# Kernel optimization log

Hardware: AMD Instinct MI355X
Metric: run time of the kernel (lower is better)

The kernel has to match this reference:

```python
import jax, jax.numpy as jnp
import numpy as np

B, S, E, H = 4, 2048, 1024, 16
D = E // H  # d_k = 64
NEG = -1000000000.0  # matches torch masked_fill constant


def setup_inputs() -> dict:
    rk = jax.random.key(0)
    kq, kk, kv, km = jax.random.split(rk, 4)
    query = jax.random.normal(kq, (B, S, E), dtype=jnp.float32)
    key = jax.random.normal(kk, (B, S, E), dtype=jnp.float32)
    value = jax.random.normal(kv, (B, S, E), dtype=jnp.float32)
    mask = jax.random.randint(km, (B, S, S), 0, 2, dtype=jnp.int32)
    return {"query": query, "key": key, "value": value, "mask": mask}


def _split_heads(x):
    # (B, S, E) -> (B, H, S, D)
    return x.reshape(B, S, H, D).transpose(0, 2, 1, 3)


def reference(query, key, value, mask):
    q = _split_heads(query)
    k = _split_heads(key)
    v = _split_heads(value)
    scale = np.float32(1.0 / np.sqrt(D))
    scores = jnp.einsum('bhqd,bhkd->bhqk', q, k) * scale  # (B,H,S,S)
    scores = jnp.where(mask[:, None, :, :] == 0, jnp.float32(NEG), scores)
    weights = jax.nn.softmax(scores, axis=-1)
    attn = jnp.einsum('bhqk,bhkd->bhqd', weights, v)  # (B,H,S,D)
    concat = attn.transpose(0, 2, 1, 3).reshape(B, S, E)
    return concat
```

## Files before the change

### kernel.cpp

```cpp
#include <hip/hip_runtime.h>
#include <hip/hip_bf16.h>
#include <math.h>

constexpr int B = 4, S = 2048, E = 1024, H = 16, D = 64;
constexpr float NEGF = -1000000000.0f;
constexpr float KSCALE = 0.125f * 1.44269504f;

typedef __attribute__((ext_vector_type(8))) short short8;
typedef __attribute__((ext_vector_type(16))) float f32x16;

__device__ inline short f2bf(float x) {
    __hip_bfloat16 h = __float2bfloat16(x);
    return *reinterpret_cast<short*>(&h);
}
__device__ inline unsigned pk(float a, float b) {
    return (unsigned)(unsigned short)f2bf(a) | ((unsigned)(unsigned short)f2bf(b) << 16);
}
__device__ inline void gl_lds16(const void* g, void* l) {
    __builtin_amdgcn_global_load_lds(
        (const __attribute__((address_space(1))) unsigned int*)g,
        (__attribute__((address_space(3))) unsigned int*)l, 16, 0, 0);
}

constexpr size_t WS_K  = 0;
constexpr size_t WS_VT = 18874368;
constexpr size_t WS_MB = 37748736;
constexpr size_t WS_NEED = 39845888;

__global__ void prep_k(const float* __restrict__ K, char* __restrict__ ws) {
    int g = blockIdx.x * 256 + threadIdx.x;
    int rowd = g >> 2, qtr = g & 3;
    int b = rowd >> 15, h = (rowd >> 11) & 15, s = rowd & 2047;
    const float* p = K + ((size_t)(b * S + s)) * E + h * 64 + qtr * 16;
    float4 v0 = *(const float4*)(p + 0),  v1 = *(const float4*)(p + 4);
    float4 v2 = *(const float4*)(p + 8),  v3 = *(const float4*)(p + 12);
    uint4 o0, o1;
    o0.x = pk(v0.x * KSCALE, v0.y * KSCALE); o0.y = pk(v0.z * KSCALE, v0.w * KSCALE);
    o0.z = pk(v1.x * KSCALE, v1.y * KSCALE); o0.w = pk(v1.z * KSCALE, v1.w * KSCALE);
    o1.x = pk(v2.x * KSCALE, v2.y * KSCALE); o1.y = pk(v2.z * KSCALE, v2.w * KSCALE);
    o1.z = pk(v3.x * KSCALE, v3.y * KSCALE); o1.w = pk(v3.z * KSCALE, v3.w * KSCALE);
    char* d = ws + WS_K + (size_t)rowd * 144 + qtr * 32;
    *(uint4*)d = o0; *(uint4*)(d + 16) = o1;
}

__global__ void prep_v(const float* __restrict__ V, char* __restrict__ ws) {
    __shared__ float Vf[64][69];
    const int tid = threadIdx.x;
    int bh = blockIdx.x >> 5, kt = blockIdx.x & 31;
    int b = bh >> 4, h = bh & 15;
    {
        int r = tid >> 2, c4 = (tid & 3) * 16;
        const float* p = V + ((size_t)(b * S + kt * 64 + r)) * E + h * 64 + c4;
        float4 a = *(const float4*)(p + 0), bb = *(const float4*)(p + 4);
        float4 c = *(const float4*)(p + 8), dd = *(const float4*)(p + 12);
        *(float4*)&Vf[r][c4 + 0] = a;  *(float4*)&Vf[r][c4 + 4] = bb;
        *(float4*)&Vf[r][c4 + 8] = c;  *(float4*)&Vf[r][c4 + 12] = dd;
    }
    __syncthreads();
    int d = tid >> 2, sq = (tid & 3) * 16;
    float v[16];
#pragma unroll
    for (int i = 0; i < 16; ++i) v[i] = Vf[sq + i][d];
    uint4 o0, o1;
    o0.x = pk(v[0], v[1]);   o0.y = pk(v[2], v[3]);
    o0.z = pk(v[4], v[5]);   o0.w = pk(v[6], v[7]);
    o1.x = pk(v[8], v[9]);   o1.y = pk(v[10], v[11]);
    o1.z = pk(v[12], v[13]); o1.w = pk(v[14], v[15]);
    char* o = ws + WS_VT + ((size_t)(bh * 32 + kt)) * 9216 + d * 144 + sq * 2;
    *(uint4*)o = o0; *(uint4*)(o + 16) = o1;
}

__global__ void prep_m(const int* __restrict__ M, unsigned long long* __restrict__ Mb) {
    const int lane = threadIdx.x & 63;
    const int wid = blockIdx.x * 4 + (threadIdx.x >> 6);
#pragma unroll
    for (int it = 0; it < 8; ++it) {
        const size_t base = ((size_t)wid * 8 + it) * 256;
        int4 mv = *(const int4*)(M + base + lane * 4);
        unsigned nib = (mv.x != 0 ? 1u : 0u) | (mv.y != 0 ? 2u : 0u)
                     | (mv.z != 0 ? 4u : 0u) | (mv.w != 0 ? 8u : 0u);
        unsigned s1 = nib | ((unsigned)__shfl_xor((int)nib, 1, 64) << 4);
        unsigned s2 = s1 | ((unsigned)__shfl_xor((int)s1, 2, 64) << 8);
        unsigned s3 = s2 | ((unsigned)__shfl_xor((int)s2, 4, 64) << 16);
        unsigned hi = (unsigned)__shfl_xor((int)s3, 8, 64);
        if ((lane & 15) == 0) {
            unsigned long long wv = (unsigned long long)s3 | ((unsigned long long)hi << 32);
            Mb[base / 64 + (lane >> 4)] = wv;
        }
    }
}

__global__ __launch_bounds__(256, 2)
void fa_mfma(const float* __restrict__ Q, const char* __restrict__ ws,
             const unsigned long long* __restrict__ Mb, float* __restrict__ O) {
    __shared__ char smem[36864];
    const int tid = threadIdx.x;
    const int w = tid >> 6, lane = tid & 63;
    const int L5 = lane & 31, h6 = lane >> 5;
    const int sh4 = h6 * 4;
    const int h = blockIdx.x & 15, b = (blockIdx.x >> 4) & 3, qt = blockIdx.x >> 6;
    const int bh = b * 16 + h;
    const int q0w = qt * 256 + w * 64;

    const char* Kws  = ws + WS_K;
    const char* Vtws = ws + WS_VT;

    short8 qf[2][4];
#pragma unroll
    for (int nb = 0; nb < 2; ++nb)
#pragma unroll
        for (int ks = 0; ks < 4; ++ks) {
            const float* qp = Q + ((size_t)(b * S + q0w + nb * 32 + L5)) * E
                                + h * 64 + ks * 16 + h6 * 8;
            float4 a = *(const float4*)qp;
            float4 c = *(const float4*)(qp + 4);
            uint4 u;
            u.x = pk(a.x, a.y); u.y = pk(a.z, a.w);
            u.z = pk(c.x, c.y); u.w = pk(c.z, c.w);
            qf[nb][ks] = *(short8*)&u;
        }

    f32x16 acc[2][2];
#pragma unroll
    for (int mb = 0; mb < 2; ++mb)
#pragma unroll
        for (int nb = 0; nb < 2; ++nb) acc[mb][nb] = (f32x16)0.0f;
    float l0 = 0.0f, l1 = 0.0f;
    const int qA = q0w + L5, qB = qA + 32;

    {
        const char* ksrc = Kws + ((size_t)bh * S) * 144;
        const char* vsrc = Vtws + ((size_t)bh * 32) * 9216;
#pragma unroll
        for (int c = 0; c < 5; ++c) {
            int idx = c * 4 + w;
            if (idx < 18) {
                int off = idx * 1024;
                const char* g = (off < 9216) ? (ksrc + off) : (vsrc + off - 9216);
                gl_lds16(g + lane * 16, smem + off);
            }
        }
    }

    for (int ti = 0; ti < 32; ++ti) {
        __syncthreads();

        if (ti + 1 < 32) {
            const char* ksrc = Kws + ((size_t)bh * S + (ti + 1) * 64) * 144;
            const char* vsrc = Vtws + ((size_t)(bh * 32 + ti + 1)) * 9216;
            char* dst = smem + ((ti + 1) & 1) * 18432;
#pragma unroll
            for (int c = 0; c < 5; ++c) {
                int idx = c * 4 + w;
                if (idx < 18) {
                    int off = idx * 1024;
                    const char* g = (off < 9216) ? (ksrc + off) : (vsrc + off - 9216);
                    gl_lds16(g + lane * 16, dst + off);
                }
            }
        }
        const unsigned long long mA = Mb[((size_t)b * S + qA) * 32 + ti];
        const unsigned long long mB = Mb[((size_t)b * S + qB) * 32 + ti];

        const char* Ks = smem + (ti & 1) * 18432;
        const char* Vt = Ks + 9216;

#pragma unroll
        for (int mbK = 0; mbK < 2; ++mbK) {
            short8 kf[4];
#pragma unroll
            for (int ks = 0; ks < 4; ++ks)
                kf[ks] = *(const short8*)(Ks + (mbK * 32 + L5) * 144 + ks * 32 + h6 * 16);
            const unsigned wmA = (unsigned)(mA >> (mbK * 32)) >> sh4;
            const unsigned wmB = (unsigned)(mB >> (mbK * 32)) >> sh4;

            short8 pf[2][2];
#pragma unroll
            for (int nb = 0; nb < 2; ++nb) {
                f32x16 s = (f32x16)0.0f;
#pragma unroll
                for (int ks = 0; ks < 4; ++ks)
                    s = __builtin_amdgcn_mfma_f32_32x32x16_bf16(kf[ks], qf[nb][ks], s, 0, 0, 0);
                const unsigned wm = nb ? wmB : wmA;
                float lacc = 0.0f;
                unsigned pd[8];
#pragma unroll
                for (int i = 0; i < 8; ++i) {
                    const int r0i = 2 * i, r1i = 2 * i + 1;
                    const int kc0 = (r0i & 3) + 8 * (r0i >> 2);
                    const int kc1 = (r1i & 3) + 8 * (r1i >> 2);
                    float e0 = __builtin_amdgcn_exp2f(((wm >> kc0) & 1u) ? s[r0i] : NEGF);
                    float e1 = __builtin_amdgcn_exp2f(((wm >> kc1) & 1u) ? s[r1i] : NEGF);
                    lacc += e0 + e1;
                    pd[i] = pk(e0, e1);
                }
                if (nb) l1 += lacc; else l0 += lacc;
#pragma unroll
                for (int sub = 0; sub < 2; ++sub) {
                    const unsigned dA = pd[4 * sub + 0], dB = pd[4 * sub + 1];
                    const unsigned dC = pd[4 * sub + 2], dD = pd[4 * sub + 3];
                    const unsigned t0 = h6 ? dA : dC;
                    const unsigned t1 = h6 ? dB : dD;
                    const unsigned r0 = (unsigned)__shfl_xor((int)t0, 32, 64);
                    const unsigned r1 = (unsigned)__shfl_xor((int)t1, 32, 64);
                    uint4 u;
                    u.x = h6 ? r0 : dA;  u.y = h6 ? r1 : dB;
                    u.z = h6 ? dC : r0;  u.w = h6 ? dD : r1;
                    pf[nb][sub] = *(short8*)&u;
                }
            }
#pragma unroll
            for (int mbV = 0; mbV < 2; ++mbV) {
                short8 vf[2];
#pragma unroll
                for (int sub = 0; sub < 2; ++sub)
                    vf[sub] = *(const short8*)(Vt + (mbV * 32 + L5) * 144
                                               + (mbK * 2 + sub) * 32 + h6 * 16);
#pragma unroll
                for (int nb = 0; nb < 2; ++nb)
#pragma unroll
                    for (int sub = 0; sub < 2; ++sub)
                        acc[mbV][nb] = __builtin_amdgcn_mfma_f32_32x32x16_bf16(
                            vf[sub], pf[nb][sub], acc[mbV][nb], 0, 0, 0);
            }
        }
    }

    l0 += __shfl_xor(l0, 32, 64);
    l1 += __shfl_xor(l1, 32, 64);
    const float inv[2] = {1.0f / l0, 1.0f / l1};
    __syncthreads();
    float* ep = (float*)(smem + w * 4608);
#pragma unroll
    for (int nb = 0; nb < 2; ++nb)
#pragma unroll
        for (int mb = 0; mb < 2; ++mb) {
#pragma unroll
            for (int r = 0; r < 16; ++r) {
                const int d = (r & 3) + 8 * (r >> 2) + sh4;
                ep[L5 * 36 + d] = acc[mb][nb][r] * inv[nb];
            }
            __builtin_amdgcn_s_waitcnt(0xc07f);
            const int row = lane >> 1, c = (lane & 1) * 16;
#pragma unroll
            for (int i = 0; i < 4; ++i) {
                float4 t = *(const float4*)&ep[row * 36 + c + 4 * i];
                *(float4*)(O + ((size_t)(b * S + q0w + nb * 32 + row)) * E
                             + h * 64 + mb * 32 + c + 4 * i) = t;
            }
            __builtin_amdgcn_s_waitcnt(0xc07f);
        }
}

constexpr int QT = 64, KT = 64, LD = D + 4;
constexpr float SCALE = 0.125f;
__global__ __launch_bounds__(256, 3)
void fa_fp32(const float* __restrict__ Q, const float* __restrict__ K,
             const float* __restrict__ V, const int* __restrict__ M,
             float* __restrict__ Out)
{
    __shared__ float Qs[QT][LD];
    __shared__ float Vs[KT][LD];
    __shared__ float KPs[KT][LD];
    const int tid = threadIdx.x, tx = tid & 15, ty = tid >> 4;
    const int bid = blockIdx.x;
    const int h = bid % H, b = (bid / H) % B, qt = bid / (H * B);
    const int q0 = qt * QT;
    {
        const int col = tx * 4;
#pragma unroll
        for (int i = 0; i < 4; ++i) {
            const int row = ty + i * 16;
            *(float4*)&Qs[row][col] = *(const float4*)&Q[((size_t)(b * S + q0 + row)) * E + h * D + col];
        }
    }
    const int qr0 = ty * 4, d0 = tx * 4;
    float acc[4][4] = {};
    float m_i[4], l_i[4];
#pragma unroll
    for (int j = 0; j < 4; ++j) { m_i[j] = -INFINITY; l_i[j] = 0.0f; }
    for (int kt = 0; kt < S; kt += KT) {
        __syncthreads();
        {
            const int col = tx * 4;
#pragma unroll
            for (int i = 0; i < 4; ++i) {
                const int row = ty + i * 16;
                const size_t g = ((size_t)(b * S + kt + row)) * E + h * D + col;
                *(float4*)&KPs[row][col] = *(const float4*)&K[g];
                *(float4*)&Vs[row][col] = *(const float4*)&V[g];
            }
        }
        __syncthreads();
        float s[4][4] = {};
#pragma unroll
        for (int d = 0; d < D; d += 4) {
            float4 a[4], bb[4];
#pragma unroll
            for (int j = 0; j < 4; ++j) a[j] = *(const float4*)&Qs[qr0 + j][d];
#pragma unroll
            for (int i = 0; i < 4; ++i) bb[i] = *(const float4*)&KPs[tx + 16 * i][d];
#pragma unroll
            for (int j = 0; j < 4; ++j)
#pragma unroll
                for (int i = 0; i < 4; ++i)
                    s[j][i] += a[j].x * bb[i].x + a[j].y * bb[i].y + a[j].z * bb[i].z + a[j].w * bb[i].w;
        }
#pragma unroll
        for (int j = 0; j < 4; ++j) {
            const int* mrow = &M[((size_t)b * S + (q0 + qr0 + j)) * S + kt];
#pragma unroll
            for (int i = 0; i < 4; ++i) {
                const int mk = mrow[tx + 16 * i];
                s[j][i] = mk ? s[j][i] * SCALE : NEGF;
            }
        }
#pragma unroll
        for (int j = 0; j < 4; ++j) {
            float tm = fmaxf(fmaxf(s[j][0], s[j][1]), fmaxf(s[j][2], s[j][3]));
#pragma unroll
            for (int off = 8; off; off >>= 1) tm = fmaxf(tm, __shfl_xor(tm, off, 16));
            const float nm = fmaxf(m_i[j], tm);
            const float alpha = __expf(m_i[j] - nm);
            m_i[j] = nm;
            float rs = 0.0f;
#pragma unroll
            for (int i = 0; i < 4; ++i) { const float p = __expf(s[j][i] - nm); s[j][i] = p; rs += p; }
#pragma unroll
            for (int off = 8; off; off >>= 1) rs += __shfl_xor(rs, off, 16);
            l_i[j] = l_i[j] * alpha + rs;
#pragma unroll
            for (int dd = 0; dd < 4; ++dd) acc[j][dd] *= alpha;
        }
        __syncthreads();
#pragma unroll
        for (int j = 0; j < 4; ++j)
#pragma unroll
            for (int i = 0; i < 4; ++i) KPs[qr0 + j][tx + 16 * i] = s[j][i];
        __syncthreads();
#pragma unroll 4
        for (int kk = 0; kk < KT; kk += 4) {
            float4 p[4], vv[4];
#pragma unroll
            for (int j = 0; j < 4; ++j) p[j] = *(const float4*)&KPs[qr0 + j][kk];
#pragma unroll
            for (int u = 0; u < 4; ++u) vv[u] = *(const float4*)&Vs[kk + u][d0];
#pragma unroll
            for (int j = 0; j < 4; ++j) {
                acc[j][0] += p[j].x * vv[0].x + p[j].y * vv[1].x + p[j].z * vv[2].x + p[j].w * vv[3].x;
                acc[j][1] += p[j].x * vv[0].y + p[j].y * vv[1].y + p[j].z * vv[2].y + p[j].w * vv[3].y;
                acc[j][2] += p[j].x * vv[0].z + p[j].y * vv[1].z + p[j].z * vv[2].z + p[j].w * vv[3].z;
                acc[j][3] += p[j].x * vv[0].w + p[j].y * vv[1].w + p[j].z * vv[2].w + p[j].w * vv[3].w;
            }
        }
    }
#pragma unroll
    for (int j = 0; j < 4; ++j) {
        const float iv = 1.0f / l_i[j];
        float4 r;
        r.x = acc[j][0] * iv; r.y = acc[j][1] * iv; r.z = acc[j][2] * iv; r.w = acc[j][3] * iv;
        *(float4*)&Out[((size_t)(b * S + q0 + qr0 + j)) * E + h * D + d0] = r;
    }
}

extern "C" void kernel_launch(void* const* d_in, const int* in_sizes, int n_in,
                              void* d_out, int out_size, void* d_ws, size_t ws_size,
                              hipStream_t stream) {
    (void)in_sizes; (void)n_in; (void)out_size;
    const float* q = (const float*)d_in[0];
    const float* k = (const float*)d_in[1];
    const float* v = (const float*)d_in[2];
    const int*   m = (const int*)d_in[3];
    float* out = (float*)d_out;

    if (ws_size >= WS_NEED) {
        char* ws = (char*)d_ws;
        prep_k<<<2048, 256, 0, stream>>>(k, ws);
        prep_v<<<2048, 256, 0, stream>>>(v, ws);
        prep_m<<<2048, 256, 0, stream>>>(m, (unsigned long long*)(ws + WS_MB));
        fa_mfma<<<512, 256, 0, stream>>>(q, ws,
            (const unsigned long long*)(ws + WS_MB), out);
    } else {
        fa_fp32<<<B * H * (S / QT), 256, 0, stream>>>(q, k, v, m, out);
    }
}
```

Measured before the change: 305.9 us.

## Fuse prep kernels and halve per-wave query rows to raise occupancy

Merges the three preprocessing kernels (K convert/scale, V transpose, mask bit-pack) into one launch to cut launch overhead. The attention kernel now gives each wave 32 query rows instead of 64, launches twice as many blocks and raises launch bounds to 4 blocks per SM, aiming for more waves to hide latency. It also changes masking to zero the exponent after exp2 rather than substituting NEG before it. The trade-off is that every K/V tile is now loaded into LDS by twice as many blocks, and each wave gets less MFMA work per K/V fragment read.

```diff
diff --git a/kernel.cpp b/kernel.cpp
--- a/kernel.cpp
+++ b/kernel.cpp
@@ -27,70 +27,75 @@
 constexpr size_t WS_MB = 37748736;
 constexpr size_t WS_NEED = 39845888;
 
-__global__ void prep_k(const float* __restrict__ K, char* __restrict__ ws) {
-    int g = blockIdx.x * 256 + threadIdx.x;
-    int rowd = g >> 2, qtr = g & 3;
-    int b = rowd >> 15, h = (rowd >> 11) & 15, s = rowd & 2047;
-    const float* p = K + ((size_t)(b * S + s)) * E + h * 64 + qtr * 16;
-    float4 v0 = *(const float4*)(p + 0),  v1 = *(const float4*)(p + 4);
-    float4 v2 = *(const float4*)(p + 8),  v3 = *(const float4*)(p + 12);
-    uint4 o0, o1;
-    o0.x = pk(v0.x * KSCALE, v0.y * KSCALE); o0.y = pk(v0.z * KSCALE, v0.w * KSCALE);
-    o0.z = pk(v1.x * KSCALE, v1.y * KSCALE); o0.w = pk(v1.z * KSCALE, v1.w * KSCALE);
-    o1.x = pk(v2.x * KSCALE, v2.y * KSCALE); o1.y = pk(v2.z * KSCALE, v2.w * KSCALE);
-    o1.z = pk(v3.x * KSCALE, v3.y * KSCALE); o1.w = pk(v3.z * KSCALE, v3.w * KSCALE);
-    char* d = ws + WS_K + (size_t)rowd * 144 + qtr * 32;
-    *(uint4*)d = o0; *(uint4*)(d + 16) = o1;
-}
-
-__global__ void prep_v(const float* __restrict__ V, char* __restrict__ ws) {
+__global__ void prep_all(const float* __restrict__ K, const float* __restrict__ V,
+                         const int* __restrict__ M, char* __restrict__ ws) {
     __shared__ float Vf[64][69];
-    const int tid = threadIdx.x;
-    int bh = blockIdx.x >> 5, kt = blockIdx.x & 31;
-    int b = bh >> 4, h = bh & 15;
-    {
-        int r = tid >> 2, c4 = (tid & 3) * 16;
-        const float* p = V + ((size_t)(b * S + kt * 64 + r)) * E + h * 64 + c4;
-        float4 a = *(const float4*)(p + 0), bb = *(const float4*)(p + 4);
-        float4 c = *(const float4*)(p + 8), dd = *(const float4*)(p + 12);
-        *(float4*)&Vf[r][c4 + 0] = a;  *(float4*)&Vf[r][c4 + 4] = bb;
-        *(float4*)&Vf[r][c4 + 8] = c;  *(float4*)&Vf[r][c4 + 12] = dd;
-    }
-    __syncthreads();
-    int d = tid >> 2, sq = (tid & 3) * 16;
-    float v[16];
-#pragma unroll
-    for (int i = 0; i < 16; ++i) v[i] = Vf[sq + i][d];
-    uint4 o0, o1;
-    o0.x = pk(v[0], v[1]);   o0.y = pk(v[2], v[3]);
-    o0.z = pk(v[4], v[5]);   o0.w = pk(v[6], v[7]);
-    o1.x = pk(v[8], v[9]);   o1.y = pk(v[10], v[11]);
-    o1.z = pk(v[12], v[13]); o1.w = pk(v[14], v[15]);
-    char* o = ws + WS_VT + ((size_t)(bh * 32 + kt)) * 9216 + d * 144 + sq * 2;
-    *(uint4*)o = o0; *(uint4*)(o + 16) = o1;
-}
-
-__global__ void prep_m(const int* __restrict__ M, unsigned long long* __restrict__ Mb) {
-    const int lane = threadIdx.x & 63;
-    const int wid = blockIdx.x * 4 + (threadIdx.x >> 6);
-#pragma unroll
-    for (int it = 0; it < 8; ++it) {
-        const size_t base = ((size_t)wid * 8 + it) * 256;
-        int4 mv = *(const int4*)(M + base + lane * 4);
-        unsigned nib = (mv.x != 0 ? 1u : 0u) | (mv.y != 0 ? 2u : 0u)
-                     | (mv.z != 0 ? 4u : 0u) | (mv.w != 0 ? 8u : 0u);
-        unsigned s1 = nib | ((unsigned)__shfl_xor((int)nib, 1, 64) << 4);
-        unsigned s2 = s1 | ((unsigned)__shfl_xor((int)s1, 2, 64) << 8);
-        unsigned s3 = s2 | ((unsigned)__shfl_xor((int)s2, 4, 64) << 16);
-        unsigned hi = (unsigned)__shfl_xor((int)s3, 8, 64);
-        if ((lane & 15) == 0) {
-            unsigned long long wv = (unsigned long long)s3 | ((unsigned long long)hi << 32);
-            Mb[base / 64 + (lane >> 4)] = wv;
-        }
-    }
-}
-
-__global__ __launch_bounds__(256, 2)
+    const int bid = blockIdx.x, tid = threadIdx.x;
+
+    {
+        int g = bid * 256 + tid;
+        int rowd = g >> 2, qtr = g & 3;
+        int b = rowd >> 15, h = (rowd >> 11) & 15, s = rowd & 2047;
+        const float* p = K + ((size_t)(b * S + s)) * E + h * 64 + qtr * 16;
+        float4 v0 = *(const float4*)(p + 0),  v1 = *(const float4*)(p + 4);
+        float4 v2 = *(const float4*)(p + 8),  v3 = *(const float4*)(p + 12);
+        uint4 o0, o1;
+        o0.x = pk(v0.x * KSCALE, v0.y * KSCALE); o0.y = pk(v0.z * KSCALE, v0.w * KSCALE);
+        o0.z = pk(v1.x * KSCALE, v1.y * KSCALE); o0.w = pk(v1.z * KSCALE, v1.w * KSCALE);
+        o1.x = pk(v2.x * KSCALE, v2.y * KSCALE); o1.y = pk(v2.z * KSCALE, v2.w * KSCALE);
+        o1.z = pk(v3.x * KSCALE, v3.y * KSCALE); o1.w = pk(v3.z * KSCALE, v3.w * KSCALE);
+        char* d = ws + WS_K + (size_t)rowd * 144 + qtr * 32;
+        *(uint4*)d = o0; *(uint4*)(d + 16) = o1;
+    }
+
+    {
+        int bh = bid >> 5, kt = bid & 31;
+        int b = bh >> 4, h = bh & 15;
+        {
+            int r = tid >> 2, c4 = (tid & 3) * 16;
+            const float* p = V + ((size_t)(b * S + kt * 64 + r)) * E + h * 64 + c4;
+            float4 a = *(const float4*)(p + 0), bb = *(const float4*)(p + 4);
+            float4 c = *(const float4*)(p + 8), dd = *(const float4*)(p + 12);
+            *(float4*)&Vf[r][c4 + 0] = a;  *(float4*)&Vf[r][c4 + 4] = bb;
+            *(float4*)&Vf[r][c4 + 8] = c;  *(float4*)&Vf[r][c4 + 12] = dd;
+        }
+        __syncthreads();
+        int d = tid >> 2, sq = (tid & 3) * 16;
+        float v[16];
+#pragma unroll
+        for (int i = 0; i < 16; ++i) v[i] = Vf[sq + i][d];
+        uint4 o0, o1;
+        o0.x = pk(v[0], v[1]);   o0.y = pk(v[2], v[3]);
+        o0.z = pk(v[4], v[5]);   o0.w = pk(v[6], v[7]);
+        o1.x = pk(v[8], v[9]);   o1.y = pk(v[10], v[11]);
+        o1.z = pk(v[12], v[13]); o1.w = pk(v[14], v[15]);
+        char* o = ws + WS_VT + ((size_t)(bh * 32 + kt)) * 9216 + d * 144 + sq * 2;
+        *(uint4*)o = o0; *(uint4*)(o + 16) = o1;
+    }
+
+    {
+        unsigned long long* Mb = (unsigned long long*)(ws + WS_MB);
+        const int lane = tid & 63;
+        const int wid = bid * 4 + (tid >> 6);
+#pragma unroll
+        for (int it = 0; it < 8; ++it) {
+            const size_t base = ((size_t)wid * 8 + it) * 256;
+            int4 mv = *(const int4*)(M + base + lane * 4);
+            unsigned nib = (mv.x != 0 ? 1u : 0u) | (mv.y != 0 ? 2u : 0u)
+                         | (mv.z != 0 ? 4u : 0u) | (mv.w != 0 ? 8u : 0u);
+            unsigned s1 = nib | ((unsigned)__shfl_xor((int)nib, 1, 64) << 4);
+            unsigned s2 = s1 | ((unsigned)__shfl_xor((int)s1, 2, 64) << 8);
+            unsigned s3 = s2 | ((unsigned)__shfl_xor((int)s2, 4, 64) << 16);
+            unsigned hi = (unsigned)__shfl_xor((int)s3, 8, 64);
+            if ((lane & 15) == 0) {
+                unsigned long long wv = (unsigned long long)s3 | ((unsigned long long)hi << 32);
+                Mb[base / 64 + (lane >> 4)] = wv;
+            }
+        }
+    }
+}
+
+__global__ __launch_bounds__(256, 4)
 void fa_mfma(const float* __restrict__ Q, const char* __restrict__ ws,
              const unsigned long long* __restrict__ Mb, float* __restrict__ O) {
     __shared__ char smem[36864];
@@ -100,33 +105,29 @@
     const int sh4 = h6 * 4;
     const int h = blockIdx.x & 15, b = (blockIdx.x >> 4) & 3, qt = blockIdx.x >> 6;
     const int bh = b * 16 + h;
-    const int q0w = qt * 256 + w * 64;
+    const int q0w = qt * 128 + w * 32;
 
     const char* Kws  = ws + WS_K;
     const char* Vtws = ws + WS_VT;
 
-    short8 qf[2][4];
-#pragma unroll
-    for (int nb = 0; nb < 2; ++nb)
-#pragma unroll
-        for (int ks = 0; ks < 4; ++ks) {
-            const float* qp = Q + ((size_t)(b * S + q0w + nb * 32 + L5)) * E
-                                + h * 64 + ks * 16 + h6 * 8;
-            float4 a = *(const float4*)qp;
-            float4 c = *(const float4*)(qp + 4);
-            uint4 u;
-            u.x = pk(a.x, a.y); u.y = pk(a.z, a.w);
-            u.z = pk(c.x, c.y); u.w = pk(c.z, c.w);
-            qf[nb][ks] = *(short8*)&u;
-        }
-
-    f32x16 acc[2][2];
-#pragma unroll
-    for (int mb = 0; mb < 2; ++mb)
-#pragma unroll
-        for (int nb = 0; nb < 2; ++nb) acc[mb][nb] = (f32x16)0.0f;
-    float l0 = 0.0f, l1 = 0.0f;
-    const int qA = q0w + L5, qB = qA + 32;
+    short8 qf[4];
+#pragma unroll
+    for (int ks = 0; ks < 4; ++ks) {
+        const float* qp = Q + ((size_t)(b * S + q0w + L5)) * E
+                            + h * 64 + ks * 16 + h6 * 8;
+        float4 a = *(const float4*)qp;
+        float4 c = *(const float4*)(qp + 4);
+        uint4 u;
+        u.x = pk(a.x, a.y); u.y = pk(a.z, a.w);
+        u.z = pk(c.x, c.y); u.w = pk(c.z, c.w);
+        qf[ks] = *(short8*)&u;
+    }
+
+    f32x16 acc[2];
+#pragma unroll
+    for (int mb = 0; mb < 2; ++mb) acc[mb] = (f32x16)0.0f;
+    float l0 = 0.0f;
+    const int qA = q0w + L5;
 
     {
         const char* ksrc = Kws + ((size_t)bh * S) * 144;
@@ -160,7 +161,6 @@
             }
         }
         const unsigned long long mA = Mb[((size_t)b * S + qA) * 32 + ti];
-        const unsigned long long mB = Mb[((size_t)b * S + qB) * 32 + ti];
 
         const char* Ks = smem + (ti & 1) * 18432;
         const char* Vt = Ks + 9216;
@@ -171,85 +171,78 @@
 #pragma unroll
             for (int ks = 0; ks < 4; ++ks)
                 kf[ks] = *(const short8*)(Ks + (mbK * 32 + L5) * 144 + ks * 32 + h6 * 16);
-            const unsigned wmA = (unsigned)(mA >> (mbK * 32)) >> sh4;
-            const unsigned wmB = (unsigned)(mB >> (mbK * 32)) >> sh4;
-
-            short8 pf[2][2];
-#pragma unroll
-            for (int nb = 0; nb < 2; ++nb) {
-                f32x16 s = (f32x16)0.0f;
-#pragma unroll
-                for (int ks = 0; ks < 4; ++ks)
-                    s = __builtin_amdgcn_mfma_f32_32x32x16_bf16(kf[ks], qf[nb][ks], s, 0, 0, 0);
-                const unsigned wm = nb ? wmB : wmA;
-                float lacc = 0.0f;
-                unsigned pd[8];
-#pragma unroll
-                for (int i = 0; i < 8; ++i) {
-                    const int r0i = 2 * i, r1i = 2 * i + 1;
-                    const int kc0 = (r0i & 3) + 8 * (r0i >> 2);
-                    const int kc1 = (r1i & 3) + 8 * (r1i >> 2);
-                    float e0 = __builtin_amdgcn_exp2f(((wm >> kc0) & 1u) ? s[r0i] : NEGF);
-                    float e1 = __builtin_amdgcn_exp2f(((wm >> kc1) & 1u) ? s[r1i] : NEGF);
-                    lacc += e0 + e1;
-                    pd[i] = pk(e0, e1);
+            const unsigned wm = (unsigned)(mA >> (mbK * 32)) >> sh4;
+
+            f32x16 s = (f32x16)0.0f;
+#pragma unroll
+            for (int ks = 0; ks < 4; ++ks)
+                s = __builtin_amdgcn_mfma_f32_32x32x16_bf16(kf[ks], qf[ks], s, 0, 0, 0);
+
+            float lacc = 0.0f;
+            unsigned pd[8];
+#pragma unroll
+            for (int i = 0; i < 8; ++i) {
+                const int r0i = 2 * i, r1i = 2 * i + 1;
+                const int kc0 = (r0i & 3) + 8 * (r0i >> 2);
+                const int kc1 = (r1i & 3) + 8 * (r1i >> 2);
+                float e0 = __builtin_amdgcn_exp2f(s[r0i]);
+                float e1 = __builtin_amdgcn_exp2f(s[r1i]);
+                e0 = ((wm >> kc0) & 1u) ? e0 : 0.0f;
+                e1 = ((wm >> kc1) & 1u) ? e1 : 0.0f;
+                lacc += e0 + e1;
+                pd[i] = pk(e0, e1);
+            }
+            l0 += lacc;
+
+            short8 pf[2];
+#pragma unroll
+            for (int sub = 0; sub < 2; ++sub) {
+                const unsigned dA = pd[4 * sub + 0], dB = pd[4 * sub + 1];
+                const unsigned dC = pd[4 * sub + 2], dD = pd[4 * sub + 3];
+                const unsigned t0 = h6 ? dA : dC;
+                const unsigned t1 = h6 ? dB : dD;
+                const unsigned r0 = (unsigned)__shfl_xor((int)t0, 32, 64);
+                const unsigned r1 = (unsigned)__shfl_xor((int)t1, 32, 64);
+                uint4 u;
+                u.x = h6 ? r0 : dA;  u.y = h6 ? r1 : dB;
+                u.z = h6 ? dC : r0;  u.w = h6 ? dD : r1;
+                pf[sub] = *(short8*)&u;
+            }
+
+#pragma unroll
+            for (int mbV = 0; mbV < 2; ++mbV) {
+#pragma unroll
+                for (int sub = 0; sub < 2; ++sub) {
+                    short8 vf = *(const short8*)(Vt + (mbV * 32 + L5) * 144
+                                                 + (mbK * 2 + sub) * 32 + h6 * 16);
+                    acc[mbV] = __builtin_amdgcn_mfma_f32_32x32x16_bf16(
+                        vf, pf[sub], acc[mbV], 0, 0, 0);
                 }
-                if (nb) l1 += lacc; else l0 += lacc;
-#pragma unroll
-                for (int sub = 0; sub < 2; ++sub) {
-                    const unsigned dA = pd[4 * sub + 0], dB = pd[4 * sub + 1];
-                    const unsigned dC = pd[4 * sub + 2], dD = pd[4 * sub + 3];
-                    const unsigned t0 = h6 ? dA : dC;
-                    const unsigned t1 = h6 ? dB : dD;
-                    const unsigned r0 = (unsigned)__shfl_xor((int)t0, 32, 64);
-                    const unsigned r1 = (unsigned)__shfl_xor((int)t1, 32, 64);
-                    uint4 u;
-                    u.x = h6 ? r0 : dA;  u.y = h6 ? r1 : dB;
-                    u.z = h6 ? dC : r0;  u.w = h6 ? dD : r1;
-                    pf[nb][sub] = *(short8*)&u;
-                }
-            }
-#pragma unroll
-            for (int mbV = 0; mbV < 2; ++mbV) {
-                short8 vf[2];
-#pragma unroll
-                for (int sub = 0; sub < 2; ++sub)
-                    vf[sub] = *(const short8*)(Vt + (mbV * 32 + L5) * 144
-                                               + (mbK * 2 + sub) * 32 + h6 * 16);
-#pragma unroll
-                for (int nb = 0; nb < 2; ++nb)
-#pragma unroll
-                    for (int sub = 0; sub < 2; ++sub)
-                        acc[mbV][nb] = __builtin_amdgcn_mfma_f32_32x32x16_bf16(
-                            vf[sub], pf[nb][sub], acc[mbV][nb], 0, 0, 0);
             }
         }
     }
 
     l0 += __shfl_xor(l0, 32, 64);
-    l1 += __shfl_xor(l1, 32, 64);
-    const float inv[2] = {1.0f / l0, 1.0f / l1};
+    const float inv = 1.0f / l0;
     __syncthreads();
     float* ep = (float*)(smem + w * 4608);
 #pragma unroll
-    for (int nb = 0; nb < 2; ++nb)
-#pragma unroll
-        for (int mb = 0; mb < 2; ++mb) {
-#pragma unroll
-            for (int r = 0; r < 16; ++r) {
-                const int d = (r & 3) + 8 * (r >> 2) + sh4;
-                ep[L5 * 36 + d] = acc[mb][nb][r] * inv[nb];
-            }
-            __builtin_amdgcn_s_waitcnt(0xc07f);
-            const int row = lane >> 1, c = (lane & 1) * 16;
-#pragma unroll
-            for (int i = 0; i < 4; ++i) {
-                float4 t = *(const float4*)&ep[row * 36 + c + 4 * i];
-                *(float4*)(O + ((size_t)(b * S + q0w + nb * 32 + row)) * E
-                             + h * 64 + mb * 32 + c + 4 * i) = t;
-            }
-            __builtin_amdgcn_s_waitcnt(0xc07f);
-        }
+    for (int mb = 0; mb < 2; ++mb) {
+#pragma unroll
+        for (int r = 0; r < 16; ++r) {
+            const int d = (r & 3) + 8 * (r >> 2) + sh4;
+            ep[L5 * 36 + d] = acc[mb][r] * inv;
+        }
+        __builtin_amdgcn_s_waitcnt(0xc07f);
+        const int row = lane >> 1, c = (lane & 1) * 16;
+#pragma unroll
+        for (int i = 0; i < 4; ++i) {
+            float4 t = *(const float4*)&ep[row * 36 + c + 4 * i];
+            *(float4*)(O + ((size_t)(b * S + q0w + row)) * E
+                         + h * 64 + mb * 32 + c + 4 * i) = t;
+        }
+        __builtin_amdgcn_s_waitcnt(0xc07f);
+    }
 }
 
 constexpr int QT = 64, KT = 64, LD = D + 4;
@@ -375,10 +368,8 @@
 
     if (ws_size >= WS_NEED) {
         char* ws = (char*)d_ws;
-        prep_k<<<2048, 256, 0, stream>>>(k, ws);
-        prep_v<<<2048, 256, 0, stream>>>(v, ws);
-        prep_m<<<2048, 256, 0, stream>>>(m, (unsigned long long*)(ws + WS_MB));
-        fa_mfma<<<512, 256, 0, stream>>>(q, ws,
+        prep_all<<<2048, 256, 0, stream>>>(k, v, m, ws);
+        fa_mfma<<<1024, 256, 0, stream>>>(q, ws,
             (const unsigned long long*)(ws + WS_MB), out);
     } else {
         fa_fp32<<<B * H * (S / QT), 256, 0, stream>>>(q, k, v, m, out);
```

Result: no change. 305.0 us (-0.3%).
